# Kernel optimization log

Hardware: AMD Instinct MI355X
Metric: run time of the kernel (lower is better)

Reference implementation:

```python
import jax, jax.numpy as jnp
import numpy as np
from jax import lax

N_PER_GRAPH = 64   # nodes per graph (dest = last node)
N_GRAPHS = 8192
DEG = 8            # out-edges per non-dest node
N_FEATS = 4
NEG = -1e9         # finite stand-in for -inf (avoids inf/nan in grads)


def _build_dag_edges():
    # node i in a graph gets DEG edges to random j in (i, N-1]; acyclic -> Bellman-Ford converges
    rng = np.random.default_rng(0)
    i = np.repeat(np.arange(N_PER_GRAPH - 1), DEG)            # [ (N-1)*DEG ]
    span = N_PER_GRAPH - 1 - i
    tgt_local = i + 1 + (rng.random((N_GRAPHS, i.size)) * span).astype(np.int64)
    off = (np.arange(N_GRAPHS, dtype=np.int64) * N_PER_GRAPH)[:, None]
    src = np.broadcast_to(i[None, :], (N_GRAPHS, i.size)) + off
    tgt = tgt_local + off
    return np.stack([src.reshape(-1), tgt.reshape(-1)])       # [2, E]


def setup_inputs() -> dict:
    key = jax.random.key(0)
    k1, k2 = jax.random.split(key, 2)
    n_nodes = N_GRAPHS * N_PER_GRAPH
    edge_index = jnp.asarray(_build_dag_edges())               # [2, E] int64
    n_edges = edge_index.shape[1]
    feats = jax.random.normal(k1, (n_edges, N_FEATS), jnp.float32) * 0.5
    dest_mask = (jnp.arange(n_nodes) % N_PER_GRAPH) == (N_PER_GRAPH - 1)
    W = jax.random.normal(k2, (1, N_FEATS), jnp.float32) * 0.5  # Linear(n_feats,1).weight
    b = jnp.zeros((1,), jnp.float32)                            # Linear bias (link_constant)
    return {"feats": feats, "dest_mask": dest_mask, "edge_index": edge_index,
            "W": W, "b": b, "n_steps": N_PER_GRAPH - 1}


def reference(feats, dest_mask, edge_index, W, b, n_steps):
    # util = coeffs(feats): per-edge scalar utility, shape [E,1]
    n_nodes = dest_mask.shape[0]
    util = feats @ W.T + b                                     # [E,1]
    src, tgt = edge_index[0], edge_index[1]                    # flow='target_to_source': aggregate into src
    value0 = jnp.where(dest_mask[:, None], 0.0, NEG)           # [n_nodes,1]; dest pinned at 0

    def step(value, _):
        msg = value[tgt] + util                                # gather value_j + util per edge
        agg = jax.ops.segment_max(msg, src, num_segments=n_nodes)  # scatter-max into source nodes
        agg = jnp.maximum(agg, NEG)                            # empty segments: -inf -> NEG
        value = jnp.where(dest_mask[:, None], 0.0, agg)        # dest stays 0
        return value, None

    value, _ = lax.scan(step, value0, None, length=n_steps)    # n_steps = max nodes/graph - 1
    return value, util
```

## Files before the change

### kernel.cpp

```cpp
#include <hip/hip_runtime.h>

#define NEGV (-1.0e9f)
constexpr int NODES = 64;
constexpr int EPG   = 504;
constexpr int STEPS = 63;

__global__ __launch_bounds__(256)
void rl_sweep_kernel(const float* __restrict__ feats,
                     const int*   __restrict__ edge_tgt,
                     const float* __restrict__ Wp,
                     const float* __restrict__ bp,
                     float*       __restrict__ out_value,
                     float*       __restrict__ out_util,
                     int n_graphs, int E)
{
    const int wid  = (blockIdx.x * blockDim.x + threadIdx.x) >> 6;
    const int lane = threadIdx.x & 63;
    if (wid >= n_graphs) return;

    const float w0 = Wp[0], w1 = Wp[1], w2 = Wp[2], w3 = Wp[3];
    const float bb = bp[0];
    const unsigned eb = (unsigned)wid * (unsigned)EPG;

    int    traw[8];
    float4 f[8];
#pragma unroll
    for (int j = 7; j >= 0; --j) {
        unsigned idx = eb + (unsigned)(j * 64 + lane);
        if (idx >= (unsigned)E) idx = (unsigned)(E - 1);
        traw[j] = edge_tgt[idx];
        f[j]    = *reinterpret_cast<const float4*>(feats + (size_t)idx * 4u);
    }

    float value = (lane == NODES - 1) ? 0.0f : NEGV;
    float u[8];

#pragma unroll
    for (int r = 7; r >= 0; --r) {
        u[r] = f[r].x * w0 + f[r].y * w1 + f[r].z * w2 + f[r].w * w3 + bb;
        const int tr = (traw[r] & (NODES - 1)) << 2;

        const int hi = (r == 7) ? (STEPS - 1) : (r * 8 + 7);
#pragma unroll
        for (int i = hi; i >= r * 8; --i) {
            const int m = i & 7;

            const float vt = __int_as_float(
                __builtin_amdgcn_ds_bpermute(tr, __float_as_int(value)));
            float msg = vt + u[r];

            msg = fmaxf(msg, __int_as_float(__builtin_amdgcn_update_dpp(
                              0, __float_as_int(msg), 0xB1, 0xF, 0xF, true)));
            msg = fmaxf(msg, __int_as_float(__builtin_amdgcn_update_dpp(
                              0, __float_as_int(msg), 0x4E, 0xF, 0xF, true)));
            msg = fmaxf(msg, __int_as_float(__builtin_amdgcn_update_dpp(
                              0, __float_as_int(msg), 0x141, 0xF, 0xF, true)));

            const float red = __int_as_float(
                __builtin_amdgcn_readlane(__float_as_int(msg), 8 * m));
            value = (lane == i) ? red : value;
        }
        __builtin_amdgcn_sched_barrier(0);
    }

    __builtin_nontemporal_store(value, out_value + (size_t)wid * NODES + lane);
#pragma unroll
    for (int j = 0; j < 8; ++j) {
        const int e = j * 64 + lane;
        if (e < EPG)
            __builtin_nontemporal_store(u[j], out_util + eb + e);
    }
}

extern "C" void kernel_launch(void* const* d_in, const int* in_sizes, int n_in,
                              void* d_out, int out_size, void* d_ws, size_t ws_size,
                              hipStream_t stream)
{
    const float* feats      = (const float*)d_in[0];
    const int*   edge_index = (const int*)d_in[2];
    const float* W          = (const float*)d_in[3];
    const float* b          = (const float*)d_in[4];

    const int E        = in_sizes[0] / 4;
    const int n_nodes  = in_sizes[1];
    const int n_graphs = n_nodes / NODES;

    float* out_value = (float*)d_out;
    float* out_util  = out_value + n_nodes;
    const int* edge_tgt = edge_index + E;

    const int total = n_graphs * 64;
    const int block = 256;
    const int grid  = (total + block - 1) / block;
    rl_sweep_kernel<<<grid, block, 0, stream>>>(feats, edge_tgt, W, b,
                                                out_value, out_util, n_graphs, E);
}
```

Before: 24.78 us.

## Process four graphs per wave with double-buffered prefetch of next graph's edges

Measured after the change: 32.75 us. 32.2% more time.

```diff
diff --git a/kernel.cpp b/kernel.cpp
--- a/kernel.cpp
+++ b/kernel.cpp
@@ -4,6 +4,11 @@
 constexpr int NODES = 64;
 constexpr int EPG   = 504;
 constexpr int STEPS = 63;
+constexpr int GPW   = 4;
+
+#define DPPMAX(x, ctrl)                                                        \
+    x = fmaxf(x, __int_as_float(__builtin_amdgcn_update_dpp(                   \
+            0, __float_as_int(x), ctrl, 0xF, 0xF, true)))
 
 __global__ __launch_bounds__(256)
 void rl_sweep_kernel(const float* __restrict__ feats,
@@ -14,61 +19,73 @@
                      float*       __restrict__ out_util,
                      int n_graphs, int E)
 {
-    const int wid  = (blockIdx.x * blockDim.x + threadIdx.x) >> 6;
+    const int wave = (blockIdx.x * blockDim.x + threadIdx.x) >> 6;
     const int lane = threadIdx.x & 63;
-    if (wid >= n_graphs) return;
+    const int g0   = wave * GPW;
+    if (g0 >= n_graphs) return;
 
     const float w0 = Wp[0], w1 = Wp[1], w2 = Wp[2], w3 = Wp[3];
     const float bb = bp[0];
-    const unsigned eb = (unsigned)wid * (unsigned)EPG;
 
-    int    traw[8];
-    float4 f[8];
+    auto load_graph = [&](int g, int (&traw)[8], float4 (&f)[8]) {
 #pragma unroll
-    for (int j = 7; j >= 0; --j) {
-        unsigned idx = eb + (unsigned)(j * 64 + lane);
-        if (idx >= (unsigned)E) idx = (unsigned)(E - 1);
-        traw[j] = edge_tgt[idx];
-        f[j]    = *reinterpret_cast<const float4*>(feats + (size_t)idx * 4u);
-    }
+        for (int j = 7; j >= 0; --j) {
+            unsigned idx = (unsigned)g * (unsigned)EPG + (unsigned)(j * 64 + lane);
+            if (idx >= (unsigned)E) idx = (unsigned)(E - 1);
+            traw[j] = edge_tgt[idx];
+            f[j]    = *reinterpret_cast<const float4*>(feats + (size_t)idx * 4u);
+        }
+    };
 
-    float value = (lane == NODES - 1) ? 0.0f : NEGV;
-    float u[8];
+    auto process = [&](int g, const int (&traw)[8], const float4 (&f)[8]) {
+        const unsigned eb = (unsigned)g * (unsigned)EPG;
+        float u[8];
+#pragma unroll
+        for (int j = 7; j >= 0; --j)
+            u[j] = f[j].x * w0 + f[j].y * w1 + f[j].z * w2 + f[j].w * w3 + bb;
 
+        float value = (lane == NODES - 1) ? 0.0f : NEGV;
 #pragma unroll
-    for (int r = 7; r >= 0; --r) {
-        u[r] = f[r].x * w0 + f[r].y * w1 + f[r].z * w2 + f[r].w * w3 + bb;
-        const int tr = (traw[r] & (NODES - 1)) << 2;
-
-        const int hi = (r == 7) ? (STEPS - 1) : (r * 8 + 7);
-#pragma unroll
-        for (int i = hi; i >= r * 8; --i) {
+        for (int i = STEPS - 1; i >= 0; --i) {
+            const int r = i >> 3;
             const int m = i & 7;
+            const int tr = (traw[r] & (NODES - 1)) << 2;
 
             const float vt = __int_as_float(
                 __builtin_amdgcn_ds_bpermute(tr, __float_as_int(value)));
             float msg = vt + u[r];
-
-            msg = fmaxf(msg, __int_as_float(__builtin_amdgcn_update_dpp(
-                              0, __float_as_int(msg), 0xB1, 0xF, 0xF, true)));
-            msg = fmaxf(msg, __int_as_float(__builtin_amdgcn_update_dpp(
-                              0, __float_as_int(msg), 0x4E, 0xF, 0xF, true)));
-            msg = fmaxf(msg, __int_as_float(__builtin_amdgcn_update_dpp(
-                              0, __float_as_int(msg), 0x141, 0xF, 0xF, true)));
+            DPPMAX(msg, 0xB1);
+            DPPMAX(msg, 0x4E);
+            DPPMAX(msg, 0x141);
 
             const float red = __int_as_float(
                 __builtin_amdgcn_readlane(__float_as_int(msg), 8 * m));
             value = (lane == i) ? red : value;
         }
-        __builtin_amdgcn_sched_barrier(0);
-    }
 
-    __builtin_nontemporal_store(value, out_value + (size_t)wid * NODES + lane);
+        __builtin_nontemporal_store(value, out_value + (size_t)g * NODES + lane);
 #pragma unroll
-    for (int j = 0; j < 8; ++j) {
-        const int e = j * 64 + lane;
-        if (e < EPG)
-            __builtin_nontemporal_store(u[j], out_util + eb + e);
+        for (int j = 0; j < 8; ++j) {
+            const int e = j * 64 + lane;
+            if (e < EPG)
+                __builtin_nontemporal_store(u[j], out_util + eb + e);
+        }
+    };
+
+    int    trA[8], trB[8];
+    float4 fA[8],  fB[8];
+    load_graph(g0, trA, fA);
+#pragma unroll
+    for (int k = 0; k < GPW; ++k) {
+        const int g = g0 + k;
+        if (g < n_graphs) {
+            if (k + 1 < GPW && g + 1 < n_graphs) {
+                if (k & 1) load_graph(g + 1, trA, fA);
+                else       load_graph(g + 1, trB, fB);
+            }
+            if (k & 1) process(g, trB, fB);
+            else       process(g, trA, fA);
+        }
     }
 }
 
@@ -89,9 +106,10 @@
     float* out_util  = out_value + n_nodes;
     const int* edge_tgt = edge_index + E;
 
-    const int total = n_graphs * 64;
-    const int block = 256;
-    const int grid  = (total + block - 1) / block;
+    const int n_waves = (n_graphs + GPW - 1) / GPW;
+    const int total   = n_waves * 64;
+    const int block   = 256;
+    const int grid    = (total + block - 1) / block;
     rl_sweep_kernel<<<grid, block, 0, stream>>>(feats, edge_tgt, W, b,
                                                 out_value, out_util, n_graphs, E);
 }
```
